# Kernel tuning notes

Measured on AMD Instinct MI355X. Metric: run time of the kernel, lower is better.

Reference implementation:

```python
import jax, jax.numpy as jnp
import numpy as np

jax.config.update("jax_enable_x64", True)  # torch uses double for the scale decomposition

ACC = 23  # 'accuracy' in integer_multiply_shift_round


def _fixed_point_mul(x_int, new_scale):
    """Bit-exact integer multiply-shift-round: x * new_scale where
    new_scale = m * 2**e (frexp), m quantized to ACC-bit integer mantissa."""
    m, e = jnp.frexp(new_scale)                      # m in [0.5, 1)
    nm = jnp.round(m * (1 << ACC)).astype(jnp.int64)  # torch casts to int32 (ACC<32); int64 is a safe superset
    tmp = x_int.astype(jnp.int64) * nm                # [B,S,D] int64
    e = e.astype(jnp.int64)
    sl = jnp.maximum(e - ACC, 0)                      # left-shift amount (e - ACC >= 0 branch)
    sr = jnp.maximum(ACC - e, 0)                      # right-shift amount (sr_round_na branch)
    left = tmp << sl
    bit = (tmp < 0).astype(jnp.int64)
    nudge = (jnp.int64(1) << jnp.maximum(sr - 1, 0)) - bit   # round-half-away-from-zero nudge
    right = jnp.where(sr > 0, (tmp + nudge) >> sr, tmp)      # sr==0 -> identity (sr_round_na early return)
    return jnp.where(e - ACC >= 0, left, right)


def setup_inputs() -> dict:
    key = jax.random.key(0)
    k1, k2 = jax.random.split(key)
    B, S, D = 4, 4096, 2048
    # integer-valued pre-activations (int32 accumulators), stored as float32 holding exact ints
    x = jax.random.randint(k1, (B, S, D), -2048, 2048, dtype=jnp.int32).astype(jnp.float32)
    identity = jax.random.randint(k2, (B, S, D), -2048, 2048, dtype=jnp.int32).astype(jnp.float32)
    return {
        "x": x,
        "identity": identity,
        "pre_act_scaling_factor": jnp.array([0.004], jnp.float32),
        "identity_scaling_factor": jnp.array([0.002], jnp.float32),
        "x_min": jnp.array([-8.0], jnp.float32),   # calibrated activation range buffers
        "x_max": jnp.array([8.0], jnp.float32),
    }


def reference(x, identity, pre_act_scaling_factor, identity_scaling_factor, x_min, x_max):
    bit = 8
    n = 2 ** (bit - 1) - 1  # 127
    # symmetric_linear_quantization_params (per-tensor)
    scale = jnp.clip(jnp.maximum(jnp.abs(x_min), jnp.abs(x_max)), 1e-8, None) / n  # [1] float32
    # FixedPointMul: requantize pre_act and identity to the output scale, add, clamp
    s64 = scale.astype(jnp.float64)
    ns_x = pre_act_scaling_factor.astype(jnp.float64) / s64
    ns_id = identity_scaling_factor.astype(jnp.float64) / s64
    out = _fixed_point_mul(x.astype(jnp.int64), ns_x) + _fixed_point_mul(identity.astype(jnp.int64), ns_id)
    q = jnp.clip(out, -n - 1, n).astype(jnp.int8)  # bit_num<=8 -> int8
    # QuantAct returns dequantized activation and its scale
    return q.astype(jnp.float32) * scale.astype(jnp.float32), scale
```

## Files before the change

kernel.cpp:

```cpp
#include <hip/hip_runtime.h>
#include <math.h>

#define ACC_BITS 23

__device__ __forceinline__ long long fixed_point_mul(long long xi, long long nm, int e) {
    long long tmp = xi * nm;
    if (e - ACC_BITS >= 0) {
        return tmp << (e - ACC_BITS);
    } else {
        int sr = ACC_BITS - e;
        long long nudge = (1LL << (sr - 1)) - (long long)(tmp < 0);
        return (tmp + nudge) >> sr;
    }
}

__global__ void __launch_bounds__(256)
quantact_kernel(const float4* __restrict__ x,
                const float4* __restrict__ idn,
                const float* __restrict__ pre_sf,
                const float* __restrict__ id_sf,
                const float* __restrict__ xminp,
                const float* __restrict__ xmaxp,
                float4* __restrict__ out,
                float* __restrict__ out_scale,
                int n4, int n)
{
    float s = fmaxf(fabsf(xminp[0]), fabsf(xmaxp[0]));
    s = fmaxf(s, 1e-8f);
    float scale = s / 127.0f;

    double s64  = (double)scale;
    double ns_x = (double)pre_sf[0] / s64;
    double ns_i = (double)id_sf[0] / s64;

    int e_x, e_i;
    double m_x = frexp(ns_x, &e_x);
    double m_i = frexp(ns_i, &e_i);
    long long nm_x = (long long)rint(m_x * 8388608.0);
    long long nm_i = (long long)rint(m_i * 8388608.0);

    int tid    = blockIdx.x * blockDim.x + threadIdx.x;
    int stride = gridDim.x * blockDim.x;
    if (tid == 0) *out_scale = scale;

    for (int i = tid; i < n4; i += stride) {
        float4 xv = x[i];
        float4 iv = idn[i];
        float4 ov;

        {
            long long o = fixed_point_mul((long long)xv.x, nm_x, e_x)
                        + fixed_point_mul((long long)iv.x, nm_i, e_i);
            o = o < -128 ? -128 : (o > 127 ? 127 : o);
            ov.x = (float)(int)o * scale;
        }
        {
            long long o = fixed_point_mul((long long)xv.y, nm_x, e_x)
                        + fixed_point_mul((long long)iv.y, nm_i, e_i);
            o = o < -128 ? -128 : (o > 127 ? 127 : o);
            ov.y = (float)(int)o * scale;
        }
        {
            long long o = fixed_point_mul((long long)xv.z, nm_x, e_x)
                        + fixed_point_mul((long long)iv.z, nm_i, e_i);
            o = o < -128 ? -128 : (o > 127 ? 127 : o);
            ov.z = (float)(int)o * scale;
        }
        {
            long long o = fixed_point_mul((long long)xv.w, nm_x, e_x)
                        + fixed_point_mul((long long)iv.w, nm_i, e_i);
            o = o < -128 ? -128 : (o > 127 ? 127 : o);
            ov.w = (float)(int)o * scale;
        }

        out[i] = ov;
    }

    const float* xs  = (const float*)x;
    const float* is_ = (const float*)idn;
    float* os = (float*)out;
    for (int j = n4 * 4 + tid; j < n; j += stride) {
        long long o = fixed_point_mul((long long)xs[j], nm_x, e_x)
                    + fixed_point_mul((long long)is_[j], nm_i, e_i);
        o = o < -128 ? -128 : (o > 127 ? 127 : o);
        os[j] = (float)(int)o * scale;
    }
}

extern "C" void kernel_launch(void* const* d_in, const int* in_sizes, int n_in,
                              void* d_out, int out_size, void* d_ws, size_t ws_size,
                              hipStream_t stream) {
    const float4* x      = (const float4*)d_in[0];
    const float4* idn    = (const float4*)d_in[1];
    const float*  pre_sf = (const float*)d_in[2];
    const float*  id_sf  = (const float*)d_in[3];
    const float*  xmin   = (const float*)d_in[4];
    const float*  xmax   = (const float*)d_in[5];

    int n  = in_sizes[0];
    int n4 = n / 4;

    float* out       = (float*)d_out;
    float* out_scale = out + n;

    const int block = 256;
    int grid = 4096;
    int max_grid = (n4 + block - 1) / block;
    if (grid > max_grid) grid = max_grid;
    if (grid < 1) grid = 1;

    quantact_kernel<<<grid, block, 0, stream>>>(x, idn, pre_sf, id_sf, xmin, xmax,
                                                (float4*)out, out_scale, n4, n);
}
```

Measured before the change: 323.7 us.

## Precompute quant params in a setup kernel and add a 32-bit fast path

Moves the per-thread double-precision scale decomposition (frexp, division, rint) into a single-thread setup kernel that writes its results to workspace, which the main kernel then reads. Adds a fast path for the normal right-shift case: 32x32->64 multiplies, branch-free nudge and shift, and a clamp done on the 32-bit halves. It also unrolls the grid-stride loop by two and uses nontemporal stores. The cost is one extra kernel launch and a dependence on the parameter struct in workspace.

New measurement: 336.9 us. +4.1%, slower.

```diff
diff --git a/kernel.cpp b/kernel.cpp
--- a/kernel.cpp
+++ b/kernel.cpp
@@ -3,30 +3,20 @@
 
 #define ACC_BITS 23
 
-__device__ __forceinline__ long long fixed_point_mul(long long xi, long long nm, int e) {
-    long long tmp = xi * nm;
-    if (e - ACC_BITS >= 0) {
-        return tmp << (e - ACC_BITS);
-    } else {
-        int sr = ACC_BITS - e;
-        long long nudge = (1LL << (sr - 1)) - (long long)(tmp < 0);
-        return (tmp + nudge) >> sr;
-    }
-}
+struct QParams {
+    float     scale;
+    int       nm_x, e_x, nm_i, e_i;
+    long long nm_x64, nm_i64;
+};
 
-__global__ void __launch_bounds__(256)
-quantact_kernel(const float4* __restrict__ x,
-                const float4* __restrict__ idn,
-                const float* __restrict__ pre_sf,
-                const float* __restrict__ id_sf,
-                const float* __restrict__ xminp,
-                const float* __restrict__ xmaxp,
-                float4* __restrict__ out,
-                float* __restrict__ out_scale,
-                int n4, int n)
+__global__ void qparams_kernel(const float* __restrict__ pre_sf,
+                               const float* __restrict__ id_sf,
+                               const float* __restrict__ xminp,
+                               const float* __restrict__ xmaxp,
+                               QParams* __restrict__ p,
+                               float* __restrict__ out_scale)
 {
-    float s = fmaxf(fabsf(xminp[0]), fabsf(xmaxp[0]));
-    s = fmaxf(s, 1e-8f);
+    float s = fmaxf(fmaxf(fabsf(xminp[0]), fabsf(xmaxp[0])), 1e-8f);
     float scale = s / 127.0f;
 
     double s64  = (double)scale;
@@ -39,49 +29,128 @@
     long long nm_x = (long long)rint(m_x * 8388608.0);
     long long nm_i = (long long)rint(m_i * 8388608.0);
 
-    int tid    = blockIdx.x * blockDim.x + threadIdx.x;
-    int stride = gridDim.x * blockDim.x;
-    if (tid == 0) *out_scale = scale;
+    p->scale = scale;
+    p->nm_x = (int)nm_x;  p->e_x = e_x;
+    p->nm_i = (int)nm_i;  p->e_i = e_i;
+    p->nm_x64 = nm_x;     p->nm_i64 = nm_i;
+    *out_scale = scale;
+}
 
-    for (int i = tid; i < n4; i += stride) {
-        float4 xv = x[i];
-        float4 iv = idn[i];
-        float4 ov;
+__device__ __forceinline__ long long fixed_point_mul64(long long xi, long long nm, int e) {
+    long long tmp = xi * nm;
+    if (e - ACC_BITS >= 0) {
+        return tmp << (e - ACC_BITS);
+    } else {
+        int sr = ACC_BITS - e;
+        long long nudge = (1LL << (sr - 1)) - (long long)(tmp < 0);
+        return (tmp + nudge) >> sr;
+    }
+}
 
-        {
-            long long o = fixed_point_mul((long long)xv.x, nm_x, e_x)
-                        + fixed_point_mul((long long)iv.x, nm_i, e_i);
-            o = o < -128 ? -128 : (o > 127 ? 127 : o);
-            ov.x = (float)(int)o * scale;
+typedef float f32x4 __attribute__((ext_vector_type(4)));
+
+__global__ void __launch_bounds__(256)
+quantact_main(const f32x4* __restrict__ x,
+              const f32x4* __restrict__ idn,
+              f32x4* __restrict__ out,
+              const QParams* __restrict__ p,
+              int n4, int n)
+{
+    const float scale = p->scale;
+    const int nm_x = p->nm_x, nm_i = p->nm_i;
+    const int e_x  = p->e_x,  e_i  = p->e_i;
+    const int sr_x = ACC_BITS - e_x, sr_i = ACC_BITS - e_i;
+
+    const int tid    = blockIdx.x * blockDim.x + threadIdx.x;
+    const int stride = gridDim.x * blockDim.x;
+
+    const bool fast = (nm_x > 0) & (nm_i > 0) &
+                      (sr_x >= 1) & (sr_x <= 62) & (sr_i >= 1) & (sr_i <= 62);
+
+    if (fast) {
+        const long long Kx = 1LL << (sr_x - 1);
+        const long long Ki = 1LL << (sr_i - 1);
+
+        int i = tid;
+        for (; i + stride < n4; i += 2 * stride) {
+            f32x4 xv0 = x[i];
+            f32x4 iv0 = idn[i];
+            f32x4 xv1 = x[i + stride];
+            f32x4 iv1 = idn[i + stride];
+            f32x4 ov0, ov1;
+            #pragma unroll
+            for (int c = 0; c < 4; ++c) {
+                {
+                    int xi = (int)xv0[c];
+                    int ii = (int)iv0[c];
+                    long long tx = (long long)xi * nm_x + Kx - (long long)((unsigned)xi >> 31);
+                    long long ti = (long long)ii * nm_i + Ki - (long long)((unsigned)ii >> 31);
+                    long long o  = (tx >> sr_x) + (ti >> sr_i);
+                    int lo = (int)o, hi = (int)(o >> 32);
+                    int cl  = lo < -128 ? -128 : (lo > 127 ? 127 : lo);
+                    int sat = hi < 0 ? -128 : 127;
+                    int q   = (hi == (lo >> 31)) ? cl : sat;
+                    ov0[c] = (float)q * scale;
+                }
+                {
+                    int xi = (int)xv1[c];
+                    int ii = (int)iv1[c];
+                    long long tx = (long long)xi * nm_x + Kx - (long long)((unsigned)xi >> 31);
+                    long long ti = (long long)ii * nm_i + Ki - (long long)((unsigned)ii >> 31);
+                    long long o  = (tx >> sr_x) + (ti >> sr_i);
+                    int lo = (int)o, hi = (int)(o >> 32);
+                    int cl  = lo < -128 ? -128 : (lo > 127 ? 127 : lo);
+                    int sat = hi < 0 ? -128 : 127;
+                    int q   = (hi == (lo >> 31)) ? cl : sat;
+                    ov1[c] = (float)q * scale;
+                }
+            }
+            __builtin_nontemporal_store(ov0, &out[i]);
+            __builtin_nontemporal_store(ov1, &out[i + stride]);
         }
-        {
-            long long o = fixed_point_mul((long long)xv.y, nm_x, e_x)
-                        + fixed_point_mul((long long)iv.y, nm_i, e_i);
-            o = o < -128 ? -128 : (o > 127 ? 127 : o);
-            ov.y = (float)(int)o * scale;
+        for (; i < n4; i += stride) {
+            f32x4 xv = x[i];
+            f32x4 iv = idn[i];
+            f32x4 ov;
+            #pragma unroll
+            for (int c = 0; c < 4; ++c) {
+                int xi = (int)xv[c];
+                int ii = (int)iv[c];
+                long long tx = (long long)xi * nm_x + Kx - (long long)((unsigned)xi >> 31);
+                long long ti = (long long)ii * nm_i + Ki - (long long)((unsigned)ii >> 31);
+                long long o  = (tx >> sr_x) + (ti >> sr_i);
+                int lo = (int)o, hi = (int)(o >> 32);
+                int cl  = lo < -128 ? -128 : (lo > 127 ? 127 : lo);
+                int sat = hi < 0 ? -128 : 127;
+                int q   = (hi == (lo >> 31)) ? cl : sat;
+                ov[c] = (float)q * scale;
+            }
+            __builtin_nontemporal_store(ov, &out[i]);
         }
-        {
-            long long o = fixed_point_mul((long long)xv.z, nm_x, e_x)
-                        + fixed_point_mul((long long)iv.z, nm_i, e_i);
-            o = o < -128 ? -128 : (o > 127 ? 127 : o);
-            ov.z = (float)(int)o * scale;
+    } else {
+        const long long nm64_x = p->nm_x64, nm64_i = p->nm_i64;
+        for (int i = tid; i < n4; i += stride) {
+            f32x4 xv = x[i];
+            f32x4 iv = idn[i];
+            f32x4 ov;
+            #pragma unroll
+            for (int c = 0; c < 4; ++c) {
+                long long o = fixed_point_mul64((long long)xv[c], nm64_x, e_x)
+                            + fixed_point_mul64((long long)iv[c], nm64_i, e_i);
+                o = o < -128 ? -128 : (o > 127 ? 127 : o);
+                ov[c] = (float)(int)o * scale;
+            }
+            out[i] = ov;
         }
-        {
-            long long o = fixed_point_mul((long long)xv.w, nm_x, e_x)
-                        + fixed_point_mul((long long)iv.w, nm_i, e_i);
-            o = o < -128 ? -128 : (o > 127 ? 127 : o);
-            ov.w = (float)(int)o * scale;
-        }
-
-        out[i] = ov;
     }
 
     const float* xs  = (const float*)x;
     const float* is_ = (const float*)idn;
     float* os = (float*)out;
+    const long long nm64_x = p->nm_x64, nm64_i = p->nm_i64;
     for (int j = n4 * 4 + tid; j < n; j += stride) {
-        long long o = fixed_point_mul((long long)xs[j], nm_x, e_x)
-                    + fixed_point_mul((long long)is_[j], nm_i, e_i);
+        long long o = fixed_point_mul64((long long)xs[j], nm64_x, e_x)
+                    + fixed_point_mul64((long long)is_[j], nm64_i, e_i);
         o = o < -128 ? -128 : (o > 127 ? 127 : o);
         os[j] = (float)(int)o * scale;
     }
@@ -90,18 +159,21 @@
 extern "C" void kernel_launch(void* const* d_in, const int* in_sizes, int n_in,
                               void* d_out, int out_size, void* d_ws, size_t ws_size,
                               hipStream_t stream) {
-    const float4* x      = (const float4*)d_in[0];
-    const float4* idn    = (const float4*)d_in[1];
-    const float*  pre_sf = (const float*)d_in[2];
-    const float*  id_sf  = (const float*)d_in[3];
-    const float*  xmin   = (const float*)d_in[4];
-    const float*  xmax   = (const float*)d_in[5];
+    const f32x4* x      = (const f32x4*)d_in[0];
+    const f32x4* idn    = (const f32x4*)d_in[1];
+    const float* pre_sf = (const float*)d_in[2];
+    const float* id_sf  = (const float*)d_in[3];
+    const float* xmin   = (const float*)d_in[4];
+    const float* xmax   = (const float*)d_in[5];
 
     int n  = in_sizes[0];
     int n4 = n / 4;
 
     float* out       = (float*)d_out;
     float* out_scale = out + n;
+    QParams* p       = (QParams*)d_ws;
+
+    qparams_kernel<<<1, 1, 0, stream>>>(pre_sf, id_sf, xmin, xmax, p, out_scale);
 
     const int block = 256;
     int grid = 4096;
@@ -109,6 +181,5 @@
     if (grid > max_grid) grid = max_grid;
     if (grid < 1) grid = 1;
 
-    quantact_kernel<<<grid, block, 0, stream>>>(x, idn, pre_sf, id_sf, xmin, xmax,
-                                                (float4*)out, out_scale, n4, n);
+    quantact_main<<<grid, block, 0, stream>>>(x, idn, (f32x4*)out, p, n4, n);
 }
```
